# Kernel optimization log

Measured on AMD Instinct MI355X. Metric: run time of the kernel, lower is better.

## Reference

```python
import jax, jax.numpy as jnp
import numpy as np

D_MODEL = 2048
N_HEADS = 16
HEAD_DIM = D_MODEL // N_HEADS
D_FF = 4 * D_MODEL
BATCH = 2
SEQ = 2048
LN_EPS = 1e-5


def setup_inputs() -> dict:
    key = jax.random.key(0)
    ks = jax.random.split(key, 12)
    s = 0.02
    return {
        "x": jax.random.normal(ks[0], (BATCH, SEQ, D_MODEL), dtype=jnp.float32),
        "alibi_bias": jax.random.normal(ks[1], (N_HEADS, SEQ, SEQ), dtype=jnp.float32),
        "W_q": jax.random.normal(ks[2], (D_MODEL, D_MODEL), dtype=jnp.float32) * s,
        "W_k": jax.random.normal(ks[3], (D_MODEL, D_MODEL), dtype=jnp.float32) * s,
        "W_v": jax.random.normal(ks[4], (D_MODEL, D_MODEL), dtype=jnp.float32) * s,
        "W_o": jax.random.normal(ks[5], (D_MODEL, D_MODEL), dtype=jnp.float32) * s,
        "ln1_g": jnp.ones((D_MODEL,), dtype=jnp.float32),
        "ln1_b": jnp.zeros((D_MODEL,), dtype=jnp.float32),
        "ln2_g": jnp.ones((D_MODEL,), dtype=jnp.float32),
        "ln2_b": jnp.zeros((D_MODEL,), dtype=jnp.float32),
        "ffn_w1": jax.random.normal(ks[6], (D_MODEL, D_FF), dtype=jnp.float32) * s,
        "ffn_b1": jnp.zeros((D_FF,), dtype=jnp.float32),
        "ffn_w2": jax.random.normal(ks[7], (D_FF, D_MODEL), dtype=jnp.float32) * s,
        "ffn_b2": jnp.zeros((D_MODEL,), dtype=jnp.float32),
    }


def _layernorm(x, g, b):
    mu = jnp.mean(x, axis=-1, keepdims=True)
    var = jnp.mean(jnp.square(x - mu), axis=-1, keepdims=True)
    return (x - mu) * jax.lax.rsqrt(var + LN_EPS) * g + b


def _mha(x, alibi_bias, W_q, W_k, W_v, W_o):
    B, S, _ = x.shape
    # nn.Linear applies x @ W.T; here W_* are stored as (in, out) so plain matmul.
    q = (x @ W_q).reshape(B, S, N_HEADS, HEAD_DIM).transpose(0, 2, 1, 3)
    k = (x @ W_k).reshape(B, S, N_HEADS, HEAD_DIM).transpose(0, 2, 1, 3)
    v = (x @ W_v).reshape(B, S, N_HEADS, HEAD_DIM).transpose(0, 2, 1, 3)
    q = q / np.sqrt(HEAD_DIM).astype(np.float32)
    scores = jnp.einsum("bhqd,bhkd->bhqk", q, k)  # [B,H,S,S]
    scores = scores + alibi_bias[None]
    causal = jnp.triu(jnp.ones((S, S), dtype=bool), k=1)
    scores = jnp.where(causal, jnp.finfo(scores.dtype).min, scores)
    attn = jax.nn.softmax(scores, axis=-1)
    out = jnp.einsum("bhqk,bhkd->bhqd", attn, v)
    out = out.transpose(0, 2, 1, 3).reshape(B, S, D_MODEL)
    return out @ W_o


def reference(x, alibi_bias, W_q, W_k, W_v, W_o, ln1_g, ln1_b, ln2_g, ln2_b,
              ffn_w1, ffn_b1, ffn_w2, ffn_b2):
    # Attention block (pre-LN, residual); dropout is identity in eval mode.
    h = x + _mha(_layernorm(x, ln1_g, ln1_b), alibi_bias, W_q, W_k, W_v, W_o)
    # FFN block
    n2 = _layernorm(h, ln2_g, ln2_b)
    ffn = jax.nn.gelu(n2 @ ffn_w1 + ffn_b1, approximate=False) @ ffn_w2 + ffn_b2
    return h + ffn
```

## Files before the change

kernel.cpp:

```cpp
#include <hip/hip_runtime.h>
#include <math.h>

#define DM   2048
#define DFF  8192
#define NH   16
#define HD   128
#define SEQ  2048
#define MROWS 4096

typedef __attribute__((ext_vector_type(4))) float  f32x4;
typedef __attribute__((ext_vector_type(8))) __bf16 bf16x8;
typedef __attribute__((ext_vector_type(4))) short  short4_t;

#define VMCNT(n) asm volatile("s_waitcnt vmcnt(" #n ")" ::: "memory")
#define LGKM0()  asm volatile("s_waitcnt lgkmcnt(0)" ::: "memory")
#define SBAR()   asm volatile("s_barrier" ::: "memory")
#define SCHEDB() __builtin_amdgcn_sched_barrier(0)

__device__ inline unsigned short f2bf(float f) {
  union { float f; unsigned int u; } x; x.f = f;
  unsigned int r = x.u + 0x7FFFu + ((x.u >> 16) & 1u);
  return (unsigned short)(r >> 16);
}

__device__ inline void gload16(const void* g, void* l) {
  __builtin_amdgcn_global_load_lds(
      (const __attribute__((address_space(1))) unsigned int*)g,
      (__attribute__((address_space(3))) unsigned int*)l, 16, 0, 0);
}

__global__ __launch_bounds__(256) void ln_kernel(
    const float* __restrict__ in, const float* __restrict__ gw,
    const float* __restrict__ bw, unsigned short* __restrict__ out)
{
  const int row = blockIdx.x;
  const float* xr = in + (size_t)row * DM;
  const int t = threadIdx.x, lane = t & 63, w = t >> 6;
  float4 v0 = ((const float4*)xr)[t];
  float4 v1 = ((const float4*)xr)[t + 256];
  float s = v0.x+v0.y+v0.z+v0.w + v1.x+v1.y+v1.z+v1.w;
  float s2 = v0.x*v0.x+v0.y*v0.y+v0.z*v0.z+v0.w*v0.w
           + v1.x*v1.x+v1.y*v1.y+v1.z*v1.z+v1.w*v1.w;
  #pragma unroll
  for (int off = 32; off; off >>= 1) { s += __shfl_xor(s, off); s2 += __shfl_xor(s2, off); }
  __shared__ float rs[4], rs2[4];
  if (lane == 0) { rs[w] = s; rs2[w] = s2; }
  __syncthreads();
  s = rs[0] + rs[1] + rs[2] + rs[3];
  s2 = rs2[0] + rs2[1] + rs2[2] + rs2[3];
  const float mu = s * (1.0f / DM);
  const float var = s2 * (1.0f / DM) - mu * mu;
  const float rstd = rsqrtf(var + 1e-5f);
  float4 g0 = ((const float4*)gw)[t],     b0 = ((const float4*)bw)[t];
  float4 g1 = ((const float4*)gw)[t+256], b1 = ((const float4*)bw)[t+256];
  unsigned short* o = out + (size_t)row * DM;
  int i0 = t * 4, i1 = (t + 256) * 4;
  o[i0+0] = f2bf((v0.x-mu)*rstd*g0.x + b0.x);
  o[i0+1] = f2bf((v0.y-mu)*rstd*g0.y + b0.y);
  o[i0+2] = f2bf((v0.z-mu)*rstd*g0.z + b0.z);
  o[i0+3] = f2bf((v0.w-mu)*rstd*g0.w + b0.w);
  o[i1+0] = f2bf((v1.x-mu)*rstd*g1.x + b1.x);
  o[i1+1] = f2bf((v1.y-mu)*rstd*g1.y + b1.y);
  o[i1+2] = f2bf((v1.z-mu)*rstd*g1.z + b1.z);
  o[i1+3] = f2bf((v1.w-mu)*rstd*g1.w + b1.w);
}

__global__ void transpose_kernel(const float* __restrict__ in,
                                 unsigned short* __restrict__ out,
                                 int nrows, int ncols)
{
  __shared__ float tile[32][33];
  const int bx = blockIdx.x * 32;
  const int by = blockIdx.y * 32;
  const int tx = threadIdx.x, ty = threadIdx.y;
  #pragma unroll
  for (int i = ty; i < 32; i += 8)
    tile[i][tx] = in[(size_t)(by + i) * ncols + bx + tx];
  __syncthreads();
  #pragma unroll
  for (int i = ty; i < 32; i += 8)
    out[(size_t)(bx + i) * nrows + by + tx] = f2bf(tile[tx][i]);
}

__global__ void transpose4_kernel(const float* __restrict__ w0,
                                  const float* __restrict__ w1,
                                  const float* __restrict__ w2,
                                  const float* __restrict__ w3,
                                  unsigned short* __restrict__ out)
{
  __shared__ float tile[32][33];
  const float* srcs[4] = {w0, w1, w2, w3};
  const float* in = srcs[blockIdx.z];
  unsigned short* o = out + (size_t)blockIdx.z * DM * DM;
  const int bx = blockIdx.x * 32;
  const int by = blockIdx.y * 32;
  const int tx = threadIdx.x, ty = threadIdx.y;
  #pragma unroll
  for (int i = ty; i < 32; i += 8)
    tile[i][tx] = in[(size_t)(by + i) * DM + bx + tx];
  __syncthreads();
  #pragma unroll
  for (int i = ty; i < 32; i += 8)
    o[(size_t)(bx + i) * DM + by + tx] = f2bf(tile[tx][i]);
}

enum { EP_QKV = 0, EP_WO = 3, EP_FFN1 = 4, EP_FFN2 = 5 };

template <int MODE>
__global__ __launch_bounds__(512, 2) void gemm_kernel(
    const unsigned short* __restrict__ A,
    const unsigned short* __restrict__ Bt,
    int K, int N,
    const float* __restrict__ res,
    const float* __restrict__ bias,
    void* __restrict__ out)
{
  __shared__ unsigned short lds[2][3][8192];

  const int t = threadIdx.x;
  const int w = t >> 6, lane = t & 63;
  const int wm = w >> 2, wn = w & 3;
  const int c = lane & 15, g = lane >> 4;
  const int l3 = lane >> 3, l7 = lane & 7;
  const int cs = c & 7;

  const long bm = (long)blockIdx.x * 128;
  const long bn = (long)blockIdx.y * 256;
  const int NT = K >> 6;
  const size_t Ksz = (size_t)K;

  const int scol = (l7 ^ l3) * 8;
  const int r0a = w * 16;

  auto stA = [&](int T) {
    unsigned short* d = &lds[T & 1][0][r0a * 64];
    #pragma unroll
    for (int j = 0; j < 2; j++)
      gload16(A + (bm + r0a + j * 8 + l3) * Ksz + T * 64 + scol, d + j * 512);
  };
  auto stB = [&](int T, int nh) {
    unsigned short* d = &lds[T & 1][1 + nh][r0a * 64];
    #pragma unroll
    for (int j = 0; j < 2; j++)
      gload16(Bt + (bn + nh * 128 + r0a + j * 8 + l3) * Ksz + T * 64 + scol, d + j * 512);
  };

  f32x4 acc[2][2][2][2];
  #pragma unroll
  for (int i = 0; i < 2; i++)
    #pragma unroll
    for (int jq = 0; jq < 2; jq++)
      #pragma unroll
      for (int m = 0; m < 2; m++)
        #pragma unroll
        for (int n = 0; n < 2; n++) acc[i][jq][m][n] = (f32x4){0.f, 0.f, 0.f, 0.f};

  stA(0); stB(0, 0); stB(0, 1);
  stA(1); stB(1, 0);
  VMCNT(4);
  SBAR();

  const int arow = (wm * 64 + c) * 64;
  const int brow = (wn * 32 + c) * 64;
  const int k0o = (g ^ cs) * 8;
  const int k1o = ((4 | g) ^ cs) * 8;

  for (int T = 0; T < NT; T++) {
    const unsigned short* LA  = lds[T & 1][0];
    const unsigned short* LB0 = lds[T & 1][1];
    const unsigned short* LB1 = lds[T & 1][2];
    bf16x8 a[2][2][2], b[2][2];

    #pragma unroll
    for (int mh = 0; mh < 2; mh++)
      #pragma unroll
      for (int m = 0; m < 2; m++) {
        a[mh][m][0] = *(const bf16x8*)&LA[arow + mh * 2048 + m * 1024 + k0o];
        a[mh][m][1] = *(const bf16x8*)&LA[arow + mh * 2048 + m * 1024 + k1o];
      }
    #pragma unroll
    for (int n = 0; n < 2; n++) {
      b[n][0] = *(const bf16x8*)&LB0[brow + n * 1024 + k0o];
      b[n][1] = *(const bf16x8*)&LB0[brow + n * 1024 + k1o];
    }
    if (T + 1 < NT) stB(T + 1, 1);
    SBAR();
    LGKM0(); SCHEDB();
    __builtin_amdgcn_s_setprio(1);
    #pragma unroll
    for (int kk = 0; kk < 2; kk++)
      #pragma unroll
      for (int mh = 0; mh < 2; mh++)
        #pragma unroll
        for (int m = 0; m < 2; m++)
          #pragma unroll
          for (int n = 0; n < 2; n++)
            acc[mh][0][m][n] = __builtin_amdgcn_mfma_f32_16x16x32_bf16(a[mh][m][kk], b[n][kk], acc[mh][0][m][n], 0, 0, 0);
    __builtin_amdgcn_s_setprio(0);
    SBAR();

    #pragma unroll
    for (int n = 0; n < 2; n++) {
      b[n][0] = *(const bf16x8*)&LB1[brow + n * 1024 + k0o];
      b[n][1] = *(const bf16x8*)&LB1[brow + n * 1024 + k1o];
    }
    if (T + 2 < NT) { stA(T + 2); stB(T + 2, 0); }
    SBAR();
    LGKM0(); SCHEDB();
    __builtin_amdgcn_s_setprio(1);
    #pragma unroll
    for (int kk = 0; kk < 2; kk++)
      #pragma unroll
      for (int mh = 0; mh < 2; mh++)
        #pragma unroll
        for (int m = 0; m < 2; m++)
          #pragma unroll
          for (int n = 0; n < 2; n++)
            acc[mh][1][m][n] = __builtin_amdgcn_mfma_f32_16x16x32_bf16(a[mh][m][kk], b[n][kk], acc[mh][1][m][n], 0, 0, 0);
    __builtin_amdgcn_s_setprio(0);
    if (T + 2 < NT) { VMCNT(4); } else { VMCNT(0); }
    SBAR();
  }

  #pragma unroll
  for (int mh = 0; mh < 2; mh++)
    #pragma unroll
    for (int nh = 0; nh < 2; nh++)
      #pragma unroll
      for (int m = 0; m < 2; m++)
        #pragma unroll
        for (int n = 0; n < 2; n++) {
          const long row0 = bm + wm * 64 + mh * 32 + m * 16 + g * 4;
          const long col  = bn + nh * 128 + wn * 32 + n * 16 + c;
          #pragma unroll
          for (int r = 0; r < 4; r++) {
            const long row = row0 + r;
            float v = acc[mh][nh][m][n][r];
            if constexpr (MODE == EP_QKV) {
              const int slot = (int)(col >> 11);
              const long cc = col & 2047;
              const long hh = cc >> 7, dd = cc & 127;
              const long bb = row >> 11, ss = row & 2047;
              unsigned short* o = (unsigned short*)out;
              if (slot == 0)
                o[((bb * NH + hh) * SEQ + ss) * HD + dd] = f2bf(v * 0.08838834764831845f);
              else if (slot == 1)
                o[8388608 + ((bb * NH + hh) * SEQ + ss) * HD + dd] = f2bf(v);
              else
                o[16777216 + ((bb * NH + hh) * HD + dd) * SEQ + ss] = f2bf(v);
            } else if constexpr (MODE == EP_WO) {
              ((float*)out)[row * DM + col] = res[row * DM + col] + v;
            } else if constexpr (MODE == EP_FFN1) {
              float u = v + bias[col];
              float y = 0.7978845608028654f * (u + 0.044715f * u * u * u);
              float e = __expf(-2.0f * fabsf(y));
              float th = (1.0f - e) / (1.0f + e);
              th = (y < 0.0f) ? -th : th;
              ((unsigned short*)out)[row * (long)N + col] = f2bf(0.5f * u * (1.0f + th));
            } else {
              ((float*)out)[row * DM + col] = res[row * DM + col] + v + bias[col];
            }
          }
        }
}

__global__ __launch_bounds__(256) void attn_kernel(
    const unsigned short* __restrict__ Q,
    const unsigned short* __restrict__ Kg,
    const unsigned short* __restrict__ Vt,
    const float* __restrict__ alibi,
    unsigned short* __restrict__ Out)
{
  __shared__ unsigned short lds[2][16384];

  const int bh = blockIdx.x;
  const int h = bh & (NH - 1);
  const int b = bh >> 4;
  const int j = blockIdx.y;
  const int t = threadIdx.x;
  const int w = t >> 6;
  const int lane = t & 63;
  const int c = lane & 15, g = lane >> 4;
  const int cx = (c & 7) << 4;

  const char* KpB = (const char*)(Kg + (size_t)bh * SEQ * HD);
  const char* VpB = (const char*)(Vt + (size_t)bh * SEQ * HD);
  const unsigned short* Qp = Q + (size_t)bh * SEQ * HD;
  const float* Ah = alibi + (size_t)h * SEQ * SEQ;

  #pragma unroll 1
  for (int half = 0; half < 2; half++) {
    const int cidx = half ? (31 - j) : j;
    const int nt = cidx + 1;
    const int qb = cidx * 64;
    const int q0 = qb + w * 16, qc = q0 + c;

    bf16x8 qf[4];
    #pragma unroll
    for (int dt = 0; dt < 4; dt++)
      qf[dt] = *(const bf16x8*)(Qp + (size_t)qc * HD + dt * 32 + g * 8);

    f32x4 oacc[8];
    #pragma unroll
    for (int d = 0; d < 8; d++) oacc[d] = (f32x4){0.f, 0.f, 0.f, 0.f};
    float m_run = -1e30f, s_run = 0.f;
    const float* Ap = Ah + (size_t)qc * SEQ;

    auto stage = [&](int tt, unsigned short* dst) {
      const size_t kvo = (size_t)tt * 64;
      #pragma unroll
      for (int k = 0; k < 8; k++) {
        const int o = w * 8192 + k * 1024 + lane * 16;
        if (w < 2) {
          const int so = o ^ (((o >> 8) & 7) << 4);
          gload16(KpB + kvo * 256 + so, dst + ((w * 8192 + k * 1024) >> 1));
        } else {
          const int o2 = o - 16384;
          const int d = o2 >> 7, win = o2 & 127;
          gload16(VpB + (size_t)d * 4096 + kvo * 2 + (win ^ ((d & 7) << 4)),
                  dst + ((w * 8192 + k * 1024) >> 1));
        }
      }
    };

    stage(0, lds[0]);
    __syncthreads();
    int buf = 0;

    for (int tt = 0; tt < nt; tt++) {
      if (tt + 1 < nt) stage(tt + 1, lds[buf ^ 1]);
      const unsigned short* LK = lds[buf];
      const unsigned short* LV = lds[buf] + 8192;
      const int kv0 = tt * 64;

      f32x4 sc[4];
      #pragma unroll
      for (int st = 0; st < 4; st++) sc[st] = (f32x4){0.f, 0.f, 0.f, 0.f};
      #pragma unroll
      for (int dt = 0; dt < 4; dt++)
        #pragma unroll
        for (int st = 0; st < 4; st++) {
          bf16x8 kf = *(const bf16x8*)&LK[(st * 4096 + c * 256 + ((dt * 64 + g * 16) ^ cx)) >> 1];
          sc[st] = __builtin_amdgcn_mfma_f32_16x16x32_bf16(kf, qf[dt], sc[st], 0, 0, 0);
        }

      float4 al[4];
      #pragma unroll
      for (int st = 0; st < 4; st++) al[st] = *(const float4*)(Ap + kv0 + st * 16 + g * 4);
      float scr[16];
      #pragma unroll
      for (int st = 0; st < 4; st++) {
        scr[st*4+0] = (kv0 + st*16 + g*4 + 0 > qc) ? -1e30f : sc[st][0] + al[st].x;
        scr[st*4+1] = (kv0 + st*16 + g*4 + 1 > qc) ? -1e30f : sc[st][1] + al[st].y;
        scr[st*4+2] = (kv0 + st*16 + g*4 + 2 > qc) ? -1e30f : sc[st][2] + al[st].z;
        scr[st*4+3] = (kv0 + st*16 + g*4 + 3 > qc) ? -1e30f : sc[st][3] + al[st].w;
      }

      float tm = scr[0];
      #pragma unroll
      for (int i = 1; i < 16; i++) tm = fmaxf(tm, scr[i]);
      tm = fmaxf(tm, __shfl_xor(tm, 16));
      tm = fmaxf(tm, __shfl_xor(tm, 32));
      const float m_new = fmaxf(m_run, tm);
      const float corr = __expf(m_run - m_new);
      float pv[16]; float ps = 0.f;
      #pragma unroll
      for (int i = 0; i < 16; i++) { pv[i] = __expf(scr[i] - m_new); ps += pv[i]; }
      ps += __shfl_xor(ps, 16);
      ps += __shfl_xor(ps, 32);
      s_run = s_run * corr + ps;
      m_run = m_new;

      short4_t pf[4];
      #pragma unroll
      for (int st = 0; st < 4; st++) {
        pf[st][0] = (short)f2bf(pv[st*4+0]); pf[st][1] = (short)f2bf(pv[st*4+1]);
        pf[st][2] = (short)f2bf(pv[st*4+2]); pf[st][3] = (short)f2bf(pv[st*4+3]);
      }

      float cf[4];
      #pragma unroll
      for (int r = 0; r < 4; r++) cf[r] = __shfl(corr, g * 4 + r);

      #pragma unroll
      for (int dt = 0; dt < 8; dt++) {
        f32x4 o = oacc[dt];
        o[0] *= cf[0]; o[1] *= cf[1]; o[2] *= cf[2]; o[3] *= cf[3];
        #pragma unroll
        for (int st = 0; st < 4; st++) {
          short4_t vf = *(const short4_t*)&LV[((dt * 16 + c) * 128 + ((st * 32 + g * 8) ^ cx)) >> 1];
          o = __builtin_amdgcn_mfma_f32_16x16x16bf16_1k(pf[st], vf, o, 0, 0, 0);
        }
        oacc[dt] = o;
      }

      __syncthreads();
      buf ^= 1;
    }

    float inv[4];
    #pragma unroll
    for (int r = 0; r < 4; r++) inv[r] = 1.0f / __shfl(s_run, g * 4 + r);
    #pragma unroll
    for (int dt = 0; dt < 8; dt++)
      #pragma unroll
      for (int r = 0; r < 4; r++)
        Out[(size_t)(b * SEQ + q0 + g * 4 + r) * DM + h * HD + dt * 16 + c] =
            f2bf(oacc[dt][r] * inv[r]);
  }
}

extern "C" void kernel_launch(void* const* d_in, const int* in_sizes, int n_in,
                              void* d_out, int out_size, void* d_ws, size_t ws_size,
                              hipStream_t stream) {
  const float* x     = (const float*)d_in[0];
  const float* alibi = (const float*)d_in[1];
  const float* Wq    = (const float*)d_in[2];
  const float* Wk    = (const float*)d_in[3];
  const float* Wv    = (const float*)d_in[4];
  const float* Wo    = (const float*)d_in[5];
  const float* ln1g  = (const float*)d_in[6];
  const float* ln1b  = (const float*)d_in[7];
  const float* ln2g  = (const float*)d_in[8];
  const float* ln2b  = (const float*)d_in[9];
  const float* w1    = (const float*)d_in[10];
  const float* b1    = (const float*)d_in[11];
  const float* w2    = (const float*)d_in[12];
  const float* b2    = (const float*)d_in[13];

  char* ws = (char*)d_ws;
  float*          hbuf = (float*)(ws);
  unsigned short* xn   = (unsigned short*)(ws + (32ull  << 20));
  unsigned short* qb   = (unsigned short*)(ws + (48ull  << 20));
  unsigned short* kb   = (unsigned short*)(ws + (64ull  << 20));
  unsigned short* vt   = (unsigned short*)(ws + (80ull  << 20));
  unsigned short* ao   = (unsigned short*)(ws + (96ull  << 20));
  unsigned short* wt   = (unsigned short*)(ws + (112ull << 20));
  unsigned short* a1   = (unsigned short*)(ws + (48ull  << 20));

  dim3 blk256(256);
  dim3 blk512(512);
  dim3 tb(32, 8);

  ln_kernel<<<MROWS, blk256, 0, stream>>>(x, ln1g, ln1b, xn);

  transpose4_kernel<<<dim3(DM/32, DM/32, 4), tb, 0, stream>>>(Wq, Wk, Wv, Wo, wt);

  gemm_kernel<EP_QKV><<<dim3(MROWS/128, (3*DM)/256), blk512, 0, stream>>>(
      xn, wt, DM, 3*DM, nullptr, nullptr, qb);

  attn_kernel<<<dim3(NH * 2, 16), blk256, 0, stream>>>(qb, kb, vt, alibi, ao);

  gemm_kernel<EP_WO><<<dim3(MROWS/128, DM/256), blk512, 0, stream>>>(
      ao, wt + 3ull * DM * DM, DM, DM, x, nullptr, hbuf);

  ln_kernel<<<MROWS, blk256, 0, stream>>>(hbuf, ln2g, ln2b, xn);

  transpose_kernel<<<dim3(DFF/32, DM/32), tb, 0, stream>>>(w1, wt, DM, DFF);
  gemm_kernel<EP_FFN1><<<dim3(MROWS/128, DFF/256), blk512, 0, stream>>>(xn, wt, DM, DFF, nullptr, b1, a1);

  transpose_kernel<<<dim3(DM/32, DFF/32), tb, 0, stream>>>(w2, wt, DFF, DM);
  gemm_kernel<EP_FFN2><<<dim3(MROWS/128, DM/256), blk512, 0, stream>>>(a1, wt, DFF, DM, hbuf, b2, (float*)d_out);
}
```

Baseline: 703.4 us.

## Add 256x256-tile GEMM for QK and FFN1, split V projection out

Adds a new GEMM kernel with 256x256 output tiles, where each wave holds 8x4 MFMA accumulators. It is used for the Q/K projection and the FFN1 GEMM to raise arithmetic intensity and cut LDS/global traffic per FLOP. The V projection, with its transposed output layout, moves to a separate 128x256 launch. The main loop is also unrolled by two with explicit buffer slots, and the sched_barrier is removed. The larger tile gives fewer blocks (e.g. 256 for the QK GEMM), which risks lower occupancy or wave quantization, plus higher register pressure.

```diff
diff --git a/kernel.cpp b/kernel.cpp
--- a/kernel.cpp
+++ b/kernel.cpp
@@ -15,7 +15,6 @@
 #define VMCNT(n) asm volatile("s_waitcnt vmcnt(" #n ")" ::: "memory")
 #define LGKM0()  asm volatile("s_waitcnt lgkmcnt(0)" ::: "memory")
 #define SBAR()   asm volatile("s_barrier" ::: "memory")
-#define SCHEDB() __builtin_amdgcn_sched_barrier(0)
 
 __device__ inline unsigned short f2bf(float f) {
   union { float f; unsigned int u; } x; x.f = f;
@@ -104,10 +103,216 @@
     o[(size_t)(bx + i) * DM + by + tx] = f2bf(tile[tx][i]);
 }
 
-enum { EP_QKV = 0, EP_WO = 3, EP_FFN1 = 4, EP_FFN2 = 5 };
+enum { EPA_QK = 0, EPA_FFN1 = 1 };
+
+#define MFMA16_256(MB_, BV_, NB_)                                                 \
+    _Pragma("unroll")                                                             \
+    for (int kk = 0; kk < 2; kk++)                                                \
+      _Pragma("unroll")                                                           \
+      for (int mf = 0; mf < 4; mf++)                                              \
+        _Pragma("unroll")                                                         \
+        for (int nf = 0; nf < 2; nf++)                                            \
+          acc[(MB_) + mf][(NB_) + nf] = __builtin_amdgcn_mfma_f32_16x16x32_bf16(  \
+              a[mf][kk], BV_[nf][kk], acc[(MB_) + mf][(NB_) + nf], 0, 0, 0);
+
+#define G256_TILE(T_, S_)                                                         \
+  {                                                                               \
+    const unsigned short* Ls = lds[S_];                                           \
+    _Pragma("unroll")                                                             \
+    for (int mf = 0; mf < 4; mf++) {                                              \
+      a[mf][0] = *(const bf16x8*)&Ls[abase + mf * 1024 + xo0];                    \
+      a[mf][1] = *(const bf16x8*)&Ls[abase + mf * 1024 + xo1];                    \
+    }                                                                             \
+    _Pragma("unroll")                                                             \
+    for (int nf = 0; nf < 2; nf++) {                                              \
+      b0[nf][0] = *(const bf16x8*)&Ls[bbase + nf * 1024 + xo0];                   \
+      b0[nf][1] = *(const bf16x8*)&Ls[bbase + nf * 1024 + xo1];                   \
+    }                                                                             \
+    if ((T_) + 1 < NT) stageB((T_) + 1, 1, (S_) ^ 1);                             \
+    SBAR();                                                                       \
+    __builtin_amdgcn_s_setprio(1);                                                \
+    MFMA16_256(0, b0, 0);                                                         \
+    __builtin_amdgcn_s_setprio(0);                                                \
+    LGKM0();                                                                      \
+    SBAR();                                                                       \
+    _Pragma("unroll")                                                             \
+    for (int nf = 0; nf < 2; nf++) {                                              \
+      b1[nf][0] = *(const bf16x8*)&Ls[bbase + 2048 + nf * 1024 + xo0];            \
+      b1[nf][1] = *(const bf16x8*)&Ls[bbase + 2048 + nf * 1024 + xo1];            \
+    }                                                                             \
+    if ((T_) + 2 < NT) stageA((T_) + 2, 0, S_);                                   \
+    SBAR();                                                                       \
+    __builtin_amdgcn_s_setprio(1);                                                \
+    MFMA16_256(0, b1, 2);                                                         \
+    __builtin_amdgcn_s_setprio(0);                                                \
+    LGKM0();                                                                      \
+    SBAR();                                                                       \
+    _Pragma("unroll")                                                             \
+    for (int mf = 0; mf < 4; mf++) {                                              \
+      a[mf][0] = *(const bf16x8*)&Ls[abase + 4096 + mf * 1024 + xo0];             \
+      a[mf][1] = *(const bf16x8*)&Ls[abase + 4096 + mf * 1024 + xo1];             \
+    }                                                                             \
+    if ((T_) + 2 < NT) stageB((T_) + 2, 0, S_);                                   \
+    SBAR();                                                                       \
+    __builtin_amdgcn_s_setprio(1);                                                \
+    MFMA16_256(4, b0, 0);                                                         \
+    __builtin_amdgcn_s_setprio(0);                                                \
+    LGKM0();                                                                      \
+    SBAR();                                                                       \
+    if ((T_) + 2 < NT) stageA((T_) + 2, 1, S_);                                   \
+    __builtin_amdgcn_s_setprio(1);                                                \
+    MFMA16_256(4, b1, 2);                                                         \
+    __builtin_amdgcn_s_setprio(0);                                                \
+    if ((T_) + 2 < NT) { VMCNT(6); } else { VMCNT(0); }                           \
+    SBAR();                                                                       \
+  }
 
 template <int MODE>
-__global__ __launch_bounds__(512, 2) void gemm_kernel(
+__global__ __launch_bounds__(512, 2) void gemm256_kernel(
+    const unsigned short* __restrict__ A,
+    const unsigned short* __restrict__ Bt,
+    int K, int N,
+    const float* __restrict__ bias,
+    void* __restrict__ out)
+{
+  __shared__ unsigned short lds[2][32768];
+
+  const int t = threadIdx.x;
+  const int w = t >> 6, lane = t & 63;
+  const int wm = w >> 2, wn = w & 3;
+  const int c = lane & 15, g = lane >> 4;
+
+  const long bm = (long)blockIdx.x * 256;
+  const long bn = (long)blockIdx.y * 256;
+  const int NT = K >> 6;
+  const size_t ks = (size_t)K;
+
+  const int tr  = t >> 3;
+  const int tc8 = (t & 7) * 8;
+  const int sch = ((t & 7) ^ (tr & 7)) * 8;
+
+  auto stageA = [&](int T, int mh, int s) {
+    const int r0 = mh * 64 + tr;
+    gload16(A + (bm + r0) * ks + T * 64 + sch,       &lds[s][r0 * 64 + tc8]);
+    gload16(A + (bm + r0 + 128) * ks + T * 64 + sch, &lds[s][(r0 + 128) * 64 + tc8]);
+  };
+  auto stageB = [&](int T, int nh, int s) {
+    const int r0 = nh * 32 + (tr & 31) + (tr >> 5) * 64;
+    gload16(Bt + (bn + r0) * ks + T * 64 + sch,       &lds[s][16384 + r0 * 64 + tc8]);
+    gload16(Bt + (bn + r0 + 128) * ks + T * 64 + sch, &lds[s][16384 + (r0 + 128) * 64 + tc8]);
+  };
+
+  f32x4 acc[8][4];
+  #pragma unroll
+  for (int i = 0; i < 8; i++)
+    #pragma unroll
+    for (int j = 0; j < 4; j++) acc[i][j] = (f32x4){0.f, 0.f, 0.f, 0.f};
+
+  const int xo0 = ((0 + g) ^ (c & 7)) * 8;
+  const int xo1 = ((4 + g) ^ (c & 7)) * 8;
+  const int abase = (wm * 128 + c) * 64;
+  const int bbase = 16384 + (wn * 64 + c) * 64;
+
+  stageA(0, 0, 0); stageB(0, 0, 0); stageA(0, 1, 0); stageB(0, 1, 0);
+  stageA(1, 0, 1); stageB(1, 0, 1); stageA(1, 1, 1);
+  VMCNT(6);
+  SBAR();
+
+  bf16x8 a[4][2], b0[2][2], b1[2][2];
+
+  for (int T = 0; T < NT; T += 2) {
+    G256_TILE(T, 0);
+    G256_TILE(T + 1, 1);
+  }
+
+  #pragma unroll
+  for (int mf = 0; mf < 8; mf++) {
+    const long row0 = bm + wm * 128 + mf * 16 + g * 4;
+    #pragma unroll
+    for (int nf = 0; nf < 4; nf++) {
+      const long col = bn + wn * 64 + nf * 16 + c;
+      #pragma unroll
+      for (int r = 0; r < 4; r++) {
+        const long row = row0 + r;
+        float v = acc[mf][nf][r];
+        if constexpr (MODE == EPA_QK) {
+          const int slot = (int)(col >> 11);
+          const long cc = col & 2047;
+          const long hh = cc >> 7, dd = cc & 127;
+          const long bb = row >> 11, ss = row & 2047;
+          unsigned short* o = (unsigned short*)out;
+          if (slot == 0)
+            o[((bb * NH + hh) * SEQ + ss) * HD + dd] = f2bf(v * 0.08838834764831845f);
+          else
+            o[8388608 + ((bb * NH + hh) * SEQ + ss) * HD + dd] = f2bf(v);
+        } else {
+          float u = v + bias[col];
+          float y = 0.7978845608028654f * (u + 0.044715f * u * u * u);
+          float e = __expf(-2.0f * fabsf(y));
+          float th = (1.0f - e) / (1.0f + e);
+          th = (y < 0.0f) ? -th : th;
+          ((unsigned short*)out)[row * (long)N + col] = f2bf(0.5f * u * (1.0f + th));
+        }
+      }
+    }
+  }
+}
+
+enum { EPB_V = 0, EPB_WO = 1, EPB_FFN2 = 2 };
+
+#define MFMA16_128(NH_)                                                           \
+    _Pragma("unroll")                                                             \
+    for (int kk = 0; kk < 2; kk++)                                                \
+      _Pragma("unroll")                                                           \
+      for (int mh = 0; mh < 2; mh++)                                              \
+        _Pragma("unroll")                                                         \
+        for (int m = 0; m < 2; m++)                                               \
+          _Pragma("unroll")                                                       \
+          for (int n = 0; n < 2; n++)                                             \
+            acc[mh][NH_][m][n] = __builtin_amdgcn_mfma_f32_16x16x32_bf16(         \
+                a[mh][m][kk], b[n][kk], acc[mh][NH_][m][n], 0, 0, 0);
+
+#define G128_TILE(T_, S_)                                                         \
+  {                                                                               \
+    const unsigned short* LA  = lds[S_][0];                                       \
+    const unsigned short* LB0 = lds[S_][1];                                       \
+    const unsigned short* LB1 = lds[S_][2];                                       \
+    _Pragma("unroll")                                                             \
+    for (int mh = 0; mh < 2; mh++)                                                \
+      _Pragma("unroll")                                                           \
+      for (int m = 0; m < 2; m++) {                                               \
+        a[mh][m][0] = *(const bf16x8*)&LA[arow + mh * 2048 + m * 1024 + k0o];     \
+        a[mh][m][1] = *(const bf16x8*)&LA[arow + mh * 2048 + m * 1024 + k1o];     \
+      }                                                                           \
+    _Pragma("unroll")                                                             \
+    for (int n = 0; n < 2; n++) {                                                 \
+      b[n][0] = *(const bf16x8*)&LB0[brow + n * 1024 + k0o];                      \
+      b[n][1] = *(const bf16x8*)&LB0[brow + n * 1024 + k1o];                      \
+    }                                                                             \
+    if ((T_) + 1 < NT) stB((T_) + 1, 1, (S_) ^ 1);                                \
+    SBAR();                                                                       \
+    __builtin_amdgcn_s_setprio(1);                                                \
+    MFMA16_128(0);                                                                \
+    __builtin_amdgcn_s_setprio(0);                                                \
+    LGKM0();                                                                      \
+    SBAR();                                                                       \
+    _Pragma("unroll")                                                             \
+    for (int n = 0; n < 2; n++) {                                                 \
+      b[n][0] = *(const bf16x8*)&LB1[brow + n * 1024 + k0o];                      \
+      b[n][1] = *(const bf16x8*)&LB1[brow + n * 1024 + k1o];                      \
+    }                                                                             \
+    if ((T_) + 2 < NT) { stA((T_) + 2, S_); stB((T_) + 2, 0, S_); }               \
+    SBAR();                                                                       \
+    __builtin_amdgcn_s_setprio(1);                                                \
+    MFMA16_128(1);                                                                \
+    __builtin_amdgcn_s_setprio(0);                                                \
+    LGKM0();                                                                      \
+    if ((T_) + 2 < NT) { VMCNT(4); } else { VMCNT(0); }                           \
+    SBAR();                                                                       \
+  }
+
+template <int MODE>
+__global__ __launch_bounds__(512, 2) void gemm128_kernel(
     const unsigned short* __restrict__ A,
     const unsigned short* __restrict__ Bt,
     int K, int N,
@@ -122,7 +327,6 @@
   const int wm = w >> 2, wn = w & 3;
   const int c = lane & 15, g = lane >> 4;
   const int l3 = lane >> 3, l7 = lane & 7;
-  const int cs = c & 7;
 
   const long bm = (long)blockIdx.x * 128;
   const long bn = (long)blockIdx.y * 256;
@@ -132,14 +336,14 @@
   const int scol = (l7 ^ l3) * 8;
   const int r0a = w * 16;
 
-  auto stA = [&](int T) {
-    unsigned short* d = &lds[T & 1][0][r0a * 64];
+  auto stA = [&](int T, int s) {
+    unsigned short* d = &lds[s][0][r0a * 64];
     #pragma unroll
     for (int j = 0; j < 2; j++)
       gload16(A + (bm + r0a + j * 8 + l3) * Ksz + T * 64 + scol, d + j * 512);
   };
-  auto stB = [&](int T, int nh) {
-    unsigned short* d = &lds[T & 1][1 + nh][r0a * 64];
+  auto stB = [&](int T, int nh, int s) {
+    unsigned short* d = &lds[s][1 + nh][r0a * 64];
     #pragma unroll
     for (int j = 0; j < 2; j++)
       gload16(Bt + (bn + nh * 128 + r0a + j * 8 + l3) * Ksz + T * 64 + scol, d + j * 512);
@@ -155,71 +359,21 @@
         #pragma unroll
         for (int n = 0; n < 2; n++) acc[i][jq][m][n] = (f32x4){0.f, 0.f, 0.f, 0.f};
 
-  stA(0); stB(0, 0); stB(0, 1);
-  stA(1); stB(1, 0);
+  stA(0, 0); stB(0, 0, 0); stB(0, 1, 0);
+  stA(1, 1); stB(1, 0, 1);
   VMCNT(4);
   SBAR();
 
   const int arow = (wm * 64 + c) * 64;
   const int brow = (wn * 32 + c) * 64;
-  const int k0o = (g ^ cs) * 8;
-  const int k1o = ((4 | g) ^ cs) * 8;
-
-  for (int T = 0; T < NT; T++) {
-    const unsigned short* LA  = lds[T & 1][0];
-    const unsigned short* LB0 = lds[T & 1][1];
-    const unsigned short* LB1 = lds[T & 1][2];
-    bf16x8 a[2][2][2], b[2][2];
-
-    #pragma unroll
-    for (int mh = 0; mh < 2; mh++)
-      #pragma unroll
-      for (int m = 0; m < 2; m++) {
-        a[mh][m][0] = *(const bf16x8*)&LA[arow + mh * 2048 + m * 1024 + k0o];
-        a[mh][m][1] = *(const bf16x8*)&LA[arow + mh * 2048 + m * 1024 + k1o];
-      }
-    #pragma unroll
-    for (int n = 0; n < 2; n++) {
-      b[n][0] = *(const bf16x8*)&LB0[brow + n * 1024 + k0o];
-      b[n][1] = *(const bf16x8*)&LB0[brow + n * 1024 + k1o];
-    }
-    if (T + 1 < NT) stB(T + 1, 1);
-    SBAR();
-    LGKM0(); SCHEDB();
-    __builtin_amdgcn_s_setprio(1);
-    #pragma unroll
-    for (int kk = 0; kk < 2; kk++)
-      #pragma unroll
-      for (int mh = 0; mh < 2; mh++)
-        #pragma unroll
-        for (int m = 0; m < 2; m++)
-          #pragma unroll
-          for (int n = 0; n < 2; n++)
-            acc[mh][0][m][n] = __builtin_amdgcn_mfma_f32_16x16x32_bf16(a[mh][m][kk], b[n][kk], acc[mh][0][m][n], 0, 0, 0);
-    __builtin_amdgcn_s_setprio(0);
-    SBAR();
-
-    #pragma unroll
-    for (int n = 0; n < 2; n++) {
-      b[n][0] = *(const bf16x8*)&LB1[brow + n * 1024 + k0o];
-      b[n][1] = *(const bf16x8*)&LB1[brow + n * 1024 + k1o];
-    }
-    if (T + 2 < NT) { stA(T + 2); stB(T + 2, 0); }
-    SBAR();
-    LGKM0(); SCHEDB();
-    __builtin_amdgcn_s_setprio(1);
-    #pragma unroll
-    for (int kk = 0; kk < 2; kk++)
-      #pragma unroll
-      for (int mh = 0; mh < 2; mh++)
-        #pragma unroll
-        for (int m = 0; m < 2; m++)
-          #pragma unroll
-          for (int n = 0; n < 2; n++)
-            acc[mh][1][m][n] = __builtin_amdgcn_mfma_f32_16x16x32_bf16(a[mh][m][kk], b[n][kk], acc[mh][1][m][n], 0, 0, 0);
-    __builtin_amdgcn_s_setprio(0);
-    if (T + 2 < NT) { VMCNT(4); } else { VMCNT(0); }
-    SBAR();
+  const int k0o = (g ^ (c & 7)) * 8;
+  const int k1o = ((4 | g) ^ (c & 7)) * 8;
+
+  bf16x8 a[2][2][2], b[2][2];
+
+  for (int T = 0; T < NT; T += 2) {
+    G128_TILE(T, 0);
+    G128_TILE(T + 1, 1);
   }
 
   #pragma unroll
@@ -236,27 +390,12 @@
           for (int r = 0; r < 4; r++) {
             const long row = row0 + r;
             float v = acc[mh][nh][m][n][r];
-            if constexpr (MODE == EP_QKV) {
-              const int slot = (int)(col >> 11);
-              const long cc = col & 2047;
-              const long hh = cc >> 7, dd = cc & 127;
+            if constexpr (MODE == EPB_V) {
+              const long hh = col >> 7, dd = col & 127;
               const long bb = row >> 11, ss = row & 2047;
-              unsigned short* o = (unsigned short*)out;
-              if (slot == 0)
-                o[((bb * NH + hh) * SEQ + ss) * HD + dd] = f2bf(v * 0.08838834764831845f);
-              else if (slot == 1)
-                o[8388608 + ((bb * NH + hh) * SEQ + ss) * HD + dd] = f2bf(v);
-              else
-                o[16777216 + ((bb * NH + hh) * HD + dd) * SEQ + ss] = f2bf(v);
-            } else if constexpr (MODE == EP_WO) {
+              ((unsigned short*)out)[((bb * NH + hh) * HD + dd) * SEQ + ss] = f2bf(v);
+            } else if constexpr (MODE == EPB_WO) {
               ((float*)out)[row * DM + col] = res[row * DM + col] + v;
-            } else if constexpr (MODE == EP_FFN1) {
-              float u = v + bias[col];
-              float y = 0.7978845608028654f * (u + 0.044715f * u * u * u);
-              float e = __expf(-2.0f * fabsf(y));
-              float th = (1.0f - e) / (1.0f + e);
-              th = (y < 0.0f) ? -th : th;
-              ((unsigned short*)out)[row * (long)N + col] = f2bf(0.5f * u * (1.0f + th));
             } else {
               ((float*)out)[row * DM + col] = res[row * DM + col] + v + bias[col];
             }
@@ -443,22 +582,25 @@
   dim3 tb(32, 8);
 
   ln_kernel<<<MROWS, blk256, 0, stream>>>(x, ln1g, ln1b, xn);
-
   transpose4_kernel<<<dim3(DM/32, DM/32, 4), tb, 0, stream>>>(Wq, Wk, Wv, Wo, wt);
 
-  gemm_kernel<EP_QKV><<<dim3(MROWS/128, (3*DM)/256), blk512, 0, stream>>>(
-      xn, wt, DM, 3*DM, nullptr, nullptr, qb);
+  gemm256_kernel<EPA_QK><<<dim3(MROWS/256, (2*DM)/256), blk512, 0, stream>>>(
+      xn, wt, DM, 2*DM, nullptr, qb);
+  gemm128_kernel<EPB_V><<<dim3(MROWS/128, DM/256), blk512, 0, stream>>>(
+      xn, wt + 2ull * DM * DM, DM, DM, nullptr, nullptr, vt);
 
   attn_kernel<<<dim3(NH * 2, 16), blk256, 0, stream>>>(qb, kb, vt, alibi, ao);
 
-  gemm_kernel<EP_WO><<<dim3(MROWS/128, DM/256), blk512, 0, stream>>>(
+  gemm128_kernel<EPB_WO><<<dim3(MROWS/128, DM/256), blk512, 0, stream>>>(
       ao, wt + 3ull * DM * DM, DM, DM, x, nullptr, hbuf);
 
   ln_kernel<<<MROWS, blk256, 0, stream>>>(hbuf, ln2g, ln2b, xn);
 
   transpose_kernel<<<dim3(DFF/32, DM/32), tb, 0, stream>>>(w1, wt, DM, DFF);
-  gemm_kernel<EP_FFN1><<<dim3(MROWS/128, DFF/256), blk512, 0, stream>>>(xn, wt, DM, DFF, nullptr, b1, a1);
+  gemm256_kernel<EPA_FFN1><<<dim3(MROWS/256, DFF/256), blk512, 0, stream>>>(
+      xn, wt, DM, DFF, b1, a1);
 
   transpose_kernel<<<dim3(DM/32, DFF/32), tb, 0, stream>>>(w2, wt, DFF, DM);
-  gemm_kernel<EP_FFN2><<<dim3(MROWS/128, DM/256), blk512, 0, stream>>>(a1, wt, DFF, DM, hbuf, b2, (float*)d_out);
-}
+  gemm128_kernel<EPB_FFN2><<<dim3(MROWS/128, DM/256), blk512, 0, stream>>>(
+      a1, wt, DFF, DM, hbuf, b2, (float*)d_out);
+}
```

Measured after the change: 656.1 us. 1.07x faster.
